# Kernel optimization log

Measured on AMD Instinct MI355X. Metric: run time of the kernel, lower is better.

The kernel has to match this reference:

```python
import jax, jax.numpy as jnp
import numpy as np

D = 1024
N_HEAD = 16
EXP = 4
EPS = 1e-6


def setup_inputs() -> dict:
    key = jax.random.key(0)
    ks = jax.random.split(key, 7)
    s = 0.02
    return {
        "x": jax.random.normal(ks[0], (2, 2048, D), dtype=jnp.float32),
        "w_qkv": jax.random.normal(ks[1], (3 * D, D), dtype=jnp.float32) * s,
        "w_o": jax.random.normal(ks[2], (D, D), dtype=jnp.float32) * s,
        "w_up": jax.random.normal(ks[3], (EXP * D, D), dtype=jnp.float32) * s,
        "w_gate": jax.random.normal(ks[4], (EXP * D, D), dtype=jnp.float32) * s,
        "w_down": jax.random.normal(ks[5], (D, EXP * D), dtype=jnp.float32) * s,
        "scale1": jnp.ones((D,), dtype=jnp.float32),
        "scale2": jnp.ones((D,), dtype=jnp.float32),
    }


def rmsnorm(x, scale):
    return x / jnp.sqrt(jnp.mean(x * x, axis=-1, keepdims=True) + EPS) * scale


def attention(x, w_qkv, w_o):
    b, s, d = x.shape
    dh = d // N_HEAD
    qkv = x @ w_qkv.T  # [b,s,3d]
    q, k, v = jnp.split(qkv, 3, axis=-1)
    # [b,h,s,dh]
    q = q.reshape(b, s, N_HEAD, dh).transpose(0, 2, 1, 3)
    k = k.reshape(b, s, N_HEAD, dh).transpose(0, 2, 1, 3)
    v = v.reshape(b, s, N_HEAD, dh).transpose(0, 2, 1, 3)
    scores = jnp.einsum("bhqd,bhkd->bhqk", q, k) / jnp.sqrt(jnp.float32(dh))
    causal = jnp.tril(jnp.ones((s, s), dtype=bool))
    scores = jnp.where(causal, scores, -jnp.inf)
    attn = jax.nn.softmax(scores, axis=-1)
    out = jnp.einsum("bhqk,bhkd->bhqd", attn, v)
    out = out.transpose(0, 2, 1, 3).reshape(b, s, d)
    return out @ w_o.T


def mlp(x, w_up, w_gate, w_down):
    return (x @ w_up.T * jax.nn.silu(x @ w_gate.T)) @ w_down.T


def reference(x, w_qkv, w_o, w_up, w_gate, w_down, scale1, scale2):
    x = x + attention(rmsnorm(x, scale1), w_qkv, w_o)
    return x + mlp(rmsnorm(x, scale2), w_up, w_gate, w_down)
```

## Files before the change

### kernel.cpp

```cpp
#include <hip/hip_runtime.h>


typedef __attribute__((ext_vector_type(8))) short short8;
typedef __attribute__((ext_vector_type(4))) float floatx4;

#define EPI_NONE 0
#define EPI_RES  1
#define EPI_GATE 2
#define EPI_QKV  3

#define QSCALE 0.1803368801f

__device__ __forceinline__ float b2f(unsigned short u) {
  union { unsigned int i; float f; } c; c.i = ((unsigned int)u) << 16; return c.f;
}
__device__ __forceinline__ unsigned short f2b(float f) {
  union { float f; unsigned int u; } c; c.f = f;
  unsigned int r = 0x7fffu + ((c.u >> 16) & 1u);
  return (unsigned short)((c.u + r) >> 16);
}
__device__ __forceinline__ unsigned int f2b2(float a, float b) {
  return (unsigned int)f2b(a) | ((unsigned int)f2b(b) << 16);
}

__device__ __forceinline__ void load_lds16(const void* g, void* l) {
  __builtin_amdgcn_global_load_lds(
      (const __attribute__((address_space(1))) unsigned int*)g,
      (__attribute__((address_space(3))) unsigned int*)l, 16, 0, 0);
}

__global__ __launch_bounds__(256)
void cvt_all_kernel(const float* __restrict__ wq, const float* __restrict__ wo,
                    const float* __restrict__ wu, const float* __restrict__ wg,
                    const float* __restrict__ wd,
                    unsigned short* __restrict__ oq, unsigned short* __restrict__ oo,
                    unsigned short* __restrict__ ou, unsigned short* __restrict__ og,
                    unsigned short* __restrict__ od) {
  int i = blockIdx.x * 256 + threadIdx.x;
  const float* src; unsigned short* dst; int k;
  if (i < 786432)        { src = wq; dst = oq; k = i; }
  else if (i < 1048576)  { src = wo; dst = oo; k = i - 786432; }
  else if (i < 2097152)  { src = wu; dst = ou; k = i - 1048576; }
  else if (i < 3145728)  { src = wg; dst = og; k = i - 2097152; }
  else                   { src = wd; dst = od; k = i - 3145728; }
  float4 v = ((const float4*)src)[k];
  ushort4 o;
  o.x = f2b(v.x); o.y = f2b(v.y); o.z = f2b(v.z); o.w = f2b(v.w);
  ((ushort4*)dst)[k] = o;
}

__global__ __launch_bounds__(256)
void rmsnorm_kernel(const float* __restrict__ x,
                    const float* __restrict__ scale,
                    unsigned short* __restrict__ y) {
  const int row = blockIdx.x;
  const int tid = threadIdx.x;
  const int base = row * 1024 + tid * 4;
  float4 v = *(const float4*)(x + base);
  float ss = v.x*v.x + v.y*v.y + v.z*v.z + v.w*v.w;
#pragma unroll
  for (int d = 32; d > 0; d >>= 1) ss += __shfl_down(ss, d);
  __shared__ float red[4];
  const int wave = tid >> 6, lane = tid & 63;
  if (lane == 0) red[wave] = ss;
  __syncthreads();
  float tot = red[0] + red[1] + red[2] + red[3];
  float rs = rsqrtf(tot * (1.0f/1024.0f) + 1e-6f);
  float4 sv = *(const float4*)(scale + tid * 4);
  ushort4 o;
  o.x = f2b(v.x * rs * sv.x);
  o.y = f2b(v.y * rs * sv.y);
  o.z = f2b(v.z * rs * sv.z);
  o.w = f2b(v.w * rs * sv.w);
  *(ushort4*)(y + base) = o;
}

__global__ __launch_bounds__(256)
void rmsnorm_res2_kernel(const float* __restrict__ x,
                         const float* __restrict__ p0,
                         const float* __restrict__ p1,
                         const float* __restrict__ scale,
                         float* __restrict__ x1,
                         unsigned short* __restrict__ y) {
  const int row = blockIdx.x;
  const int tid = threadIdx.x;
  const int base = row * 1024 + tid * 4;
  float4 a = *(const float4*)(x + base);
  float4 b = *(const float4*)(p0 + base);
  float4 c = *(const float4*)(p1 + base);
  float4 v;
  v.x = a.x + b.x + c.x; v.y = a.y + b.y + c.y;
  v.z = a.z + b.z + c.z; v.w = a.w + b.w + c.w;
  *(float4*)(x1 + base) = v;
  float ss = v.x*v.x + v.y*v.y + v.z*v.z + v.w*v.w;
#pragma unroll
  for (int d = 32; d > 0; d >>= 1) ss += __shfl_down(ss, d);
  __shared__ float red[4];
  const int wave = tid >> 6, lane = tid & 63;
  if (lane == 0) red[wave] = ss;
  __syncthreads();
  float tot = red[0] + red[1] + red[2] + red[3];
  float rs = rsqrtf(tot * (1.0f/1024.0f) + 1e-6f);
  float4 sv = *(const float4*)(scale + tid * 4);
  ushort4 o;
  o.x = f2b(v.x * rs * sv.x);
  o.y = f2b(v.y * rs * sv.y);
  o.z = f2b(v.z * rs * sv.z);
  o.w = f2b(v.w * rs * sv.w);
  *(ushort4*)(y + base) = o;
}

__global__ __launch_bounds__(256)
void reduce_out_kernel(const float* __restrict__ x1,
                       const float* __restrict__ p1,
                       float* outp) {
  int i = blockIdx.x * 256 + threadIdx.x;
  float4 a = ((const float4*)x1)[i];
  float4 b = ((const float4*)p1)[i];
  float4 c = ((float4*)outp)[i];
  float4 v;
  v.x = a.x + b.x + c.x; v.y = a.y + b.y + c.y;
  v.z = a.z + b.z + c.z; v.w = a.w + b.w + c.w;
  ((float4*)outp)[i] = v;
}

template<int EPI, typename OutT, typename ResT>
__global__ __launch_bounds__(256)
void gemm_bt(const unsigned short* __restrict__ A,
             const unsigned short* __restrict__ B,
             OutT* C, const ResT* R, unsigned short* VT,
             int M, int N, int K, int ldc) {
  __shared__ __align__(16) unsigned short As[128 * 32];
  __shared__ __align__(16) unsigned short Bs[128 * 32];
  const int tid = threadIdx.x;
  const int wave = tid >> 6;
  const int lane = tid & 63;
  const int m0 = blockIdx.y * 128;
  const int n0 = blockIdx.x * 128;
  const int wm = (wave & 1) * 64;
  const int wn = (wave >> 1) * 64;
  const int frow = lane & 15;
  const int fk = (lane >> 4) * 8;

  floatx4 acc[4][4];
#pragma unroll
  for (int i = 0; i < 4; ++i)
#pragma unroll
    for (int j = 0; j < 4; ++j) acc[i][j] = (floatx4){0.f, 0.f, 0.f, 0.f};

  const int srow = lane >> 2;
  const int scol = (lane & 3) * 8;
  const unsigned short* Ag  = A + (size_t)(m0 + wave * 16 + srow) * K + scol;
  const unsigned short* Ag2 = A + (size_t)(m0 + (wave + 4) * 16 + srow) * K + scol;
  const unsigned short* Bg  = B + (size_t)(n0 + wave * 16 + srow) * K + scol;
  const unsigned short* Bg2 = B + (size_t)(n0 + (wave + 4) * 16 + srow) * K + scol;

  for (int k0 = 0; k0 < K; k0 += 32) {
    __syncthreads();
    load_lds16(Ag + k0,  &As[wave * 512]);
    load_lds16(Ag2 + k0, &As[(wave + 4) * 512]);
    load_lds16(Bg + k0,  &Bs[wave * 512]);
    load_lds16(Bg2 + k0, &Bs[(wave + 4) * 512]);
    __syncthreads();
    short8 af[4], bf[4];
#pragma unroll
    for (int i = 0; i < 4; ++i) af[i] = *(const short8*)&As[(wm + 16*i + frow)*32 + fk];
#pragma unroll
    for (int j = 0; j < 4; ++j) bf[j] = *(const short8*)&Bs[(wn + 16*j + frow)*32 + fk];
#pragma unroll
    for (int i = 0; i < 4; ++i)
#pragma unroll
      for (int j = 0; j < 4; ++j)
        acc[i][j] = __builtin_amdgcn_mfma_f32_16x16x32_bf16(af[i], bf[j], acc[i][j], 0, 0, 0);
  }

  const int g4 = (lane >> 4) * 4;

  if constexpr (EPI == EPI_QKV) {
    if (n0 >= 2048) {
#pragma unroll
      for (int i = 0; i < 4; ++i) {
        const int row0 = m0 + wm + 16*i + g4;
        const int b = row0 >> 11, s0 = row0 & 2047;
#pragma unroll
        for (int j = 0; j < 4; ++j) {
          const int col = n0 + wn + 16*j + frow;
          const int dg = col - 2048;
          const int rowv = (b << 10) + dg;
          ushort4 ov;
          ov.x = f2b(acc[i][j][0]);
          ov.y = f2b(acc[i][j][1]);
          ov.z = f2b(acc[i][j][2]);
          ov.w = f2b(acc[i][j][3]);
          *(ushort4*)(VT + (size_t)rowv * 2048 + s0) = ov;
        }
      }
      return;
    }
  }

  const float qs = (EPI == EPI_QKV && n0 < 1024) ? QSCALE : 1.0f;
#pragma unroll
  for (int i = 0; i < 4; ++i) {
#pragma unroll
    for (int r = 0; r < 4; ++r) {
      const int row = m0 + wm + 16*i + g4 + r;
#pragma unroll
      for (int j = 0; j < 4; ++j) {
        const int col = n0 + wn + 16*j + frow;
        const size_t idx = (size_t)row * ldc + col;
        float v = acc[i][j][r];
        if constexpr (EPI == EPI_RES) {
          v += (float)R[idx];
        } else if constexpr (EPI == EPI_GATE) {
          float up = b2f((unsigned short)R[idx]);
          v = up * (v / (1.f + __expf(-v)));
        } else if constexpr (EPI == EPI_QKV) {
          v *= qs;
        }
        if constexpr (sizeof(OutT) == 4) C[idx] = v;
        else                             C[idx] = f2b(v);
      }
    }
  }
}

__global__ __launch_bounds__(256)
void gemm_bt_splitk(const unsigned short* __restrict__ A,
                    const unsigned short* __restrict__ B,
                    float* __restrict__ P0, float* __restrict__ P1,
                    int M, int N, int K, int Ks) {
  __shared__ __align__(16) unsigned short As[128 * 32];
  __shared__ __align__(16) unsigned short Bs[128 * 32];
  const int tid = threadIdx.x;
  const int wave = tid >> 6;
  const int lane = tid & 63;
  const int m0 = blockIdx.y * 128;
  const int n0 = blockIdx.x * 128;
  const int z = blockIdx.z;
  float* C = z ? P1 : P0;
  const int kbase = z * Ks;
  const int wm = (wave & 1) * 64;
  const int wn = (wave >> 1) * 64;
  const int frow = lane & 15;
  const int fk = (lane >> 4) * 8;

  floatx4 acc[4][4];
#pragma unroll
  for (int i = 0; i < 4; ++i)
#pragma unroll
    for (int j = 0; j < 4; ++j) acc[i][j] = (floatx4){0.f, 0.f, 0.f, 0.f};

  const int srow = lane >> 2;
  const int scol = (lane & 3) * 8;
  const unsigned short* Ag  = A + (size_t)(m0 + wave * 16 + srow) * K + kbase + scol;
  const unsigned short* Ag2 = A + (size_t)(m0 + (wave + 4) * 16 + srow) * K + kbase + scol;
  const unsigned short* Bg  = B + (size_t)(n0 + wave * 16 + srow) * K + kbase + scol;
  const unsigned short* Bg2 = B + (size_t)(n0 + (wave + 4) * 16 + srow) * K + kbase + scol;

  for (int k0 = 0; k0 < Ks; k0 += 32) {
    __syncthreads();
    load_lds16(Ag + k0,  &As[wave * 512]);
    load_lds16(Ag2 + k0, &As[(wave + 4) * 512]);
    load_lds16(Bg + k0,  &Bs[wave * 512]);
    load_lds16(Bg2 + k0, &Bs[(wave + 4) * 512]);
    __syncthreads();
    short8 af[4], bf[4];
#pragma unroll
    for (int i = 0; i < 4; ++i) af[i] = *(const short8*)&As[(wm + 16*i + frow)*32 + fk];
#pragma unroll
    for (int j = 0; j < 4; ++j) bf[j] = *(const short8*)&Bs[(wn + 16*j + frow)*32 + fk];
#pragma unroll
    for (int i = 0; i < 4; ++i)
#pragma unroll
      for (int j = 0; j < 4; ++j)
        acc[i][j] = __builtin_amdgcn_mfma_f32_16x16x32_bf16(af[i], bf[j], acc[i][j], 0, 0, 0);
  }

  const int g4 = (lane >> 4) * 4;
#pragma unroll
  for (int i = 0; i < 4; ++i)
#pragma unroll
    for (int r = 0; r < 4; ++r) {
      const int row = m0 + wm + 16*i + g4 + r;
#pragma unroll
      for (int j = 0; j < 4; ++j) {
        const int col = n0 + wn + 16*j + frow;
        C[(size_t)row * N + col] = acc[i][j][r];
      }
    }
}


#define A_OFF(q,h) (((q)*2+(h))*8192)
#define B_OFF(q,h) (32768 + ((q)*2+(h))*8192)

#define GBAR() __builtin_amdgcn_s_barrier()
#define WLG()  asm volatile("s_waitcnt lgkmcnt(0)" ::: "memory")
#define WVM(N) asm volatile("s_waitcnt vmcnt(" #N ")" ::: "memory")

#define STAGE(LB, SRC, T) do {                                               \
    const unsigned short* _s = (SRC) + (size_t)r0 * 1024 + (T) * 64 + gs;    \
    load_lds16(_s,             &lds[(LB) + wave * 512]);                     \
    load_lds16(_s + 64 * 1024, &lds[(LB) + 4096 + wave * 512]);              \
  } while (0)

#define LDA4(dst, q, h) do {                                                 \
    const unsigned short* _b = &lds[A_OFF(q,h) + arow];                      \
    _Pragma("unroll")                                                        \
    for (int _i = 0; _i < 4; ++_i) {                                         \
      dst[_i][0] = *(const short8*)(_b + _i * 1024 + g0);                    \
      dst[_i][1] = *(const short8*)(_b + _i * 1024 + g1);                    \
    }                                                                        \
  } while (0)

#define LDB2(dst, q, h) do {                                                 \
    const unsigned short* _b = &lds[B_OFF(q,h) + brow];                      \
    _Pragma("unroll")                                                        \
    for (int _j = 0; _j < 2; ++_j) {                                         \
      dst[_j][0] = *(const short8*)(_b + _j * 1024 + g0);                    \
      dst[_j][1] = *(const short8*)(_b + _j * 1024 + g1);                    \
    }                                                                        \
  } while (0)

#define MMQ(aa, bb, IO, JO) do {                                             \
    _Pragma("unroll")                                                        \
    for (int _i = 0; _i < 4; ++_i)                                           \
      _Pragma("unroll")                                                      \
      for (int _j = 0; _j < 2; ++_j) {                                       \
        acc[(IO)+_i][(JO)+_j] = __builtin_amdgcn_mfma_f32_16x16x32_bf16(     \
            aa[_i][0], bb[_j][0], acc[(IO)+_i][(JO)+_j], 0, 0, 0);           \
        acc[(IO)+_i][(JO)+_j] = __builtin_amdgcn_mfma_f32_16x16x32_bf16(     \
            aa[_i][1], bb[_j][1], acc[(IO)+_i][(JO)+_j], 0, 0, 0);           \
      }                                                                      \
  } while (0)

__global__ __launch_bounds__(512, 2)
void gemm256_upgate(const unsigned short* __restrict__ A,
                    const unsigned short* __restrict__ Bu,
                    const unsigned short* __restrict__ Bg,
                    unsigned short* __restrict__ C) {
  extern __shared__ __align__(16) unsigned short lds[];
  const int tid  = threadIdx.x;
  const int wave = tid >> 6;
  const int lane = tid & 63;
  const int wr   = wave >> 2;
  const int wc   = wave & 3;
  const int frow = lane & 15;
  const int s4   = lane >> 4;

  const int orig = blockIdx.x;
  const int swz  = (orig & 7) * 64 + (orig >> 3);
  const int bx   = swz & 31;
  const int by   = swz >> 5;
  const int m0   = by * 256;
  const int n0   = bx * 128;

  const int f7 = frow & 7;
  const int g0 = ((0 + s4) ^ f7) * 8;
  const int g1 = ((4 + s4) ^ f7) * 8;
  const int arow = (wr * 64 + frow) * 64;
  const int brow = (wc * 32 + frow) * 64;

  const int r0 = wave * 8 + (lane >> 3);
  const int gs = ((lane & 7) ^ (lane >> 3)) * 8;

  const unsigned short* Asrc  = A  + (size_t)m0 * 1024;
  const unsigned short* B0src = Bu + (size_t)(bx * 128) * 1024;
  const unsigned short* B1src = Bg + (size_t)(bx * 128) * 1024;

  floatx4 acc[8][4];
#pragma unroll
  for (int i = 0; i < 8; ++i)
#pragma unroll
    for (int j = 0; j < 4; ++j) acc[i][j] = (floatx4){0.f, 0.f, 0.f, 0.f};

  STAGE(A_OFF(0,0), Asrc, 0);
  STAGE(B_OFF(0,0), B0src, 0);
  STAGE(B_OFF(0,1), B1src, 0);
  STAGE(A_OFF(0,1), Asrc + 128 * 1024, 0);
  WVM(4);
  STAGE(A_OFF(1,0), Asrc, 1);
  STAGE(B_OFF(1,0), B0src, 1);
  STAGE(B_OFF(1,1), B1src, 1);
  WVM(6);
  GBAR();

  short8 af0[4][2], af1[4][2], bf0[2][2], bf1[2][2];

  for (int it = 0; it < 8; ++it) {
    const int t   = it * 2;
    const int tn2 = (t + 2) & 15;
    const int tn3 = (t + 3) & 15;
    LDA4(af0, 0, 0);
    LDB2(bf0, 0, 0);
    STAGE(A_OFF(1,1), Asrc + 128 * 1024, (t + 1) & 15);
    GBAR(); WLG();
    __builtin_amdgcn_s_setprio(1); MMQ(af0, bf0, 0, 0); __builtin_amdgcn_s_setprio(0);
    GBAR();
    LDB2(bf1, 0, 1);
    STAGE(A_OFF(0,0), Asrc, tn2);
    GBAR(); WLG();
    __builtin_amdgcn_s_setprio(1); MMQ(af0, bf1, 0, 2); __builtin_amdgcn_s_setprio(0);
    GBAR();
    LDA4(af1, 0, 1);
    STAGE(B_OFF(0,0), B0src, tn2);
    GBAR(); WLG();
    __builtin_amdgcn_s_setprio(1); MMQ(af1, bf0, 4, 0); __builtin_amdgcn_s_setprio(0);
    GBAR();
    STAGE(B_OFF(0,1), B1src, tn2);
    GBAR();
    __builtin_amdgcn_s_setprio(1); MMQ(af1, bf1, 4, 2); __builtin_amdgcn_s_setprio(0);
    WVM(6);
    GBAR();
    LDA4(af0, 1, 0);
    LDB2(bf0, 1, 0);
    STAGE(A_OFF(0,1), Asrc + 128 * 1024, tn2);
    GBAR(); WLG();
    __builtin_amdgcn_s_setprio(1); MMQ(af0, bf0, 0, 0); __builtin_amdgcn_s_setprio(0);
    GBAR();
    LDB2(bf1, 1, 1);
    STAGE(A_OFF(1,0), Asrc, tn3);
    GBAR(); WLG();
    __builtin_amdgcn_s_setprio(1); MMQ(af0, bf1, 0, 2); __builtin_amdgcn_s_setprio(0);
    GBAR();
    LDA4(af1, 1, 1);
    STAGE(B_OFF(1,0), B0src, tn3);
    GBAR(); WLG();
    __builtin_amdgcn_s_setprio(1); MMQ(af1, bf0, 4, 0); __builtin_amdgcn_s_setprio(0);
    GBAR();
    STAGE(B_OFF(1,1), B1src, tn3);
    GBAR();
    __builtin_amdgcn_s_setprio(1); MMQ(af1, bf1, 4, 2); __builtin_amdgcn_s_setprio(0);
    WVM(6);
    GBAR();
  }
  asm volatile("s_waitcnt vmcnt(0)" ::: "memory");

#pragma unroll
  for (int i = 0; i < 8; ++i) {
    const int row = m0 + (i >> 2) * 128 + wr * 64 + (i & 3) * 16 + s4 * 4;
#pragma unroll
    for (int j = 0; j < 2; ++j) {
      const int col = n0 + wc * 32 + j * 16 + frow;
#pragma unroll
      for (int r = 0; r < 4; ++r) {
        const float g = acc[i][j + 2][r];
        const float v = acc[i][j][r] * (g / (1.f + __expf(-g)));
        C[(size_t)(row + r) * 4096 + col] = f2b(v);
      }
    }
  }
}

__global__ __launch_bounds__(256, 2)
void attn_kernel(const unsigned short* __restrict__ qkv,
                 const unsigned short* __restrict__ vt,
                 unsigned short* __restrict__ out) {
  const int lin = blockIdx.x;
  const int bh = lin & 31;
  const int q_idx = lin >> 5;
  const int qblk = (q_idx < 8) ? (2 * q_idx) : (31 - 2 * q_idx);
  const int b = bh >> 4, h = bh & 15;
  const int tid = threadIdx.x, w = tid >> 6, lane = tid & 63;
  const int f = lane & 15, g = lane >> 4;
  const int fk = g * 8, g4 = g * 4;

  __shared__ __align__(16) unsigned short Ks[2][128 * 32];
  __shared__ __align__(16) unsigned short Vs[4][64 * 32];
  __shared__ __align__(16) unsigned int   pl[4][64 * 36];

  const unsigned short* Qb = qkv + (size_t)(b * 2048) * 2048 + h * 64;
  const unsigned short* Kb = Qb + 1024;
  const unsigned short* Vt = vt + ((size_t)(b * 16 + h) * 64) * 2048;

  const int q0 = qblk * 128 + w * 32;
  short8 qf[2][2];
#pragma unroll
  for (int i = 0; i < 2; ++i)
#pragma unroll
    for (int kq = 0; kq < 2; ++kq)
      qf[i][kq] = *(const short8*)(Qb + (size_t)(q0 + 16*i + f) * 2048 + kq * 32 + fk);

  float m_s[2] = {-1e30f, -1e30f}, l_s[2] = {0.f, 0.f};
  floatx4 o[4][2];
#pragma unroll
  for (int mt = 0; mt < 4; ++mt)
#pragma unroll
    for (int i = 0; i < 2; ++i) o[mt][i] = (floatx4){0.f, 0.f, 0.f, 0.f};

  const int srow = lane >> 2;
  const int scol = (lane & 3) * 8;
  unsigned int* plw = pl[w];

  for (int kb = 0; kb <= qblk; ++kb) {
    __syncthreads();
#pragma unroll
    for (int u = 0; u < 2; ++u) {
      const int seg = w + 4 * u;
#pragma unroll
      for (int kq = 0; kq < 2; ++kq)
        load_lds16(Kb + (size_t)(kb * 128 + seg * 16 + srow) * 2048 + kq * 32 + scol,
                   &Ks[kq][seg * 512]);
    }
#pragma unroll
    for (int c = 0; c < 4; ++c)
      load_lds16(Vt + (size_t)(w * 16 + srow) * 2048 + kb * 128 + c * 32 + scol,
                 &Vs[c][w * 512]);
    __syncthreads();

    const bool diag = (kb == qblk);
    const int jhi0 = diag ? 2 * w : 7;
    const int jhi1 = diag ? 2 * w + 1 : 7;

    floatx4 s[8][2];
#pragma unroll
    for (int j = 0; j < 8; ++j) {
      if (j > jhi1) continue;
      short8 kf0 = *(const short8*)&Ks[0][(16*j + f) * 32 + fk];
      short8 kf1 = *(const short8*)&Ks[1][(16*j + f) * 32 + fk];
#pragma unroll
      for (int i = 0; i < 2; ++i) {
        if (j > (i ? jhi1 : jhi0)) continue;
        s[j][i] = (floatx4){0.f, 0.f, 0.f, 0.f};
        s[j][i] = __builtin_amdgcn_mfma_f32_16x16x32_bf16(kf0, qf[i][0], s[j][i], 0, 0, 0);
        s[j][i] = __builtin_amdgcn_mfma_f32_16x16x32_bf16(kf1, qf[i][1], s[j][i], 0, 0, 0);
      }
    }
    if (diag) {
#pragma unroll
      for (int i = 0; i < 2; ++i) {
        const int qo = 32 * w + 16 * i + f;
        const int jh = i ? jhi1 : jhi0;
#pragma unroll
        for (int j = 0; j < 8; ++j) {
          if (j > jh) continue;
#pragma unroll
          for (int r = 0; r < 4; ++r)
            if (16 * j + g4 + r > qo) s[j][i][r] = -1e30f;
        }
      }
    }
#pragma unroll
    for (int i = 0; i < 2; ++i) {
      const int jh = i ? jhi1 : jhi0;
      float mx = -1e30f;
#pragma unroll
      for (int j = 0; j < 8; ++j) {
        if (j > jh) continue;
#pragma unroll
        for (int r = 0; r < 4; ++r) mx = fmaxf(mx, s[j][i][r]);
      }
      mx = fmaxf(mx, __shfl_xor(mx, 16));
      mx = fmaxf(mx, __shfl_xor(mx, 32));
      const float mnew = fmaxf(m_s[i], mx);
      const float alpha = exp2f(m_s[i] - mnew);
      float rs = 0.f;
#pragma unroll
      for (int j = 0; j < 8; ++j) {
        if (j > jh) continue;
#pragma unroll
        for (int r = 0; r < 4; ++r) {
          float pv = exp2f(s[j][i][r] - mnew);
          s[j][i][r] = pv;
          rs += pv;
        }
      }
      rs += __shfl_xor(rs, 16);
      rs += __shfl_xor(rs, 32);
      l_s[i] = l_s[i] * alpha + rs;
      m_s[i] = mnew;
#pragma unroll
      for (int mt = 0; mt < 4; ++mt) o[mt][i] *= alpha;
    }
#pragma unroll
    for (int i = 0; i < 2; ++i) {
      const int jh = i ? jhi1 : jhi0;
#pragma unroll
      for (int j = 0; j < 8; ++j) {
        if (j > jh) continue;
        plw[(8*j + 2*g + 0) * 36 + 16*i + f] = f2b2(s[j][i][0], s[j][i][1]);
        plw[(8*j + 2*g + 1) * 36 + 16*i + f] = f2b2(s[j][i][2], s[j][i][3]);
      }
    }
    if (diag) {
      plw[(8*(2*w + 1) + 2*g + 0) * 36 + f] = 0u;
      plw[(8*(2*w + 1) + 2*g + 1) * 36 + f] = 0u;
    }
    const int chi = diag ? w : 3;
#pragma unroll
    for (int c = 0; c < 4; ++c) {
      if (c > chi) continue;
      union { unsigned int d[4]; short8 v; } pb[2];
#pragma unroll
      for (int i = 0; i < 2; ++i)
#pragma unroll
        for (int k = 0; k < 4; ++k)
          pb[i].d[k] = plw[(16*c + 4*g + k) * 36 + 16*i + f];
#pragma unroll
      for (int mt = 0; mt < 4; ++mt) {
        short8 va = *(const short8*)&Vs[c][(16*mt + f) * 32 + fk];
#pragma unroll
        for (int i = 0; i < 2; ++i)
          o[mt][i] = __builtin_amdgcn_mfma_f32_16x16x32_bf16(va, pb[i].v, o[mt][i], 0, 0, 0);
      }
    }
  }

#pragma unroll
  for (int i = 0; i < 2; ++i) {
    const float inv = 1.0f / l_s[i];
    unsigned short* orow = out + (size_t)(b * 2048 + q0 + 16*i + f) * 1024 + h * 64;
#pragma unroll
    for (int mt = 0; mt < 4; ++mt) {
      ushort4 ov;
      ov.x = f2b(o[mt][i][0] * inv);
      ov.y = f2b(o[mt][i][1] * inv);
      ov.z = f2b(o[mt][i][2] * inv);
      ov.w = f2b(o[mt][i][3] * inv);
      *(ushort4*)(orow + 16 * mt + g4) = ov;
    }
  }
}

extern "C" void kernel_launch(void* const* d_in, const int* in_sizes, int n_in,
                              void* d_out, int out_size, void* d_ws, size_t ws_size,
                              hipStream_t stream) {
  const float* x      = (const float*)d_in[0];
  const float* w_qkv  = (const float*)d_in[1];
  const float* w_o    = (const float*)d_in[2];
  const float* w_up   = (const float*)d_in[3];
  const float* w_gate = (const float*)d_in[4];
  const float* w_down = (const float*)d_in[5];
  const float* scale1 = (const float*)d_in[6];
  const float* scale2 = (const float*)d_in[7];

  char* ws = (char*)d_ws;
  unsigned short* wq_b = (unsigned short*)(ws);
  unsigned short* wo_b = (unsigned short*)(ws +  6291456);
  unsigned short* wu_b = (unsigned short*)(ws +  8388608);
  unsigned short* wg_b = (unsigned short*)(ws + 16777216);
  unsigned short* wd_b = (unsigned short*)(ws + 25165824);
  unsigned short* qkv  = (unsigned short*)(ws + 33554432);
  unsigned short* hup  = (unsigned short*)(ws + 33554432);
  unsigned short* vT   = (unsigned short*)(ws + 50331648);
  unsigned short* attnb= (unsigned short*)(ws + 58720256);
  unsigned short* xn   = (unsigned short*)(ws + 67108864);
  float*          x1   = (float*)         (ws + 75497472);
  float*          outp = (float*)d_out;

  float* wo_p0   = (float*)(ws + 33554432);
  float* wo_p1   = (float*)d_out;
  float* down_p0 = (float*)d_out;
  float* down_p1 = (float*)(ws + 8388608);

  const int M = 4096;
  dim3 blk(256);

  static int lds_opted = 0;
  if (!lds_opted) {
    hipFuncSetAttribute((const void*)gemm256_upgate,
                        hipFuncAttributeMaxDynamicSharedMemorySize, 131072);
    lds_opted = 1;
  }

  cvt_all_kernel<<<16384, blk, 0, stream>>>(w_qkv, w_o, w_up, w_gate, w_down,
                                            wq_b, wo_b, wu_b, wg_b, wd_b);

  rmsnorm_kernel<<<4096, blk, 0, stream>>>(x, scale1, xn);
  gemm_bt<EPI_QKV, unsigned short, unsigned short>
      <<<dim3(24, 32), blk, 0, stream>>>(xn, wq_b, qkv, (const unsigned short*)nullptr, vT,
                                         M, 3072, 1024, 2048);
  attn_kernel<<<dim3(512), blk, 0, stream>>>(qkv, vT, attnb);
  gemm_bt_splitk<<<dim3(8, 32, 2), blk, 0, stream>>>(attnb, wo_b, wo_p0, wo_p1,
                                                     M, 1024, 1024, 512);

  rmsnorm_res2_kernel<<<4096, blk, 0, stream>>>(x, wo_p0, wo_p1, scale2, x1, xn);

  gemm256_upgate<<<dim3(512), dim3(512), 131072, stream>>>(xn, wu_b, wg_b, hup);
  gemm_bt_splitk<<<dim3(8, 32, 2), blk, 0, stream>>>(hup, wd_b, down_p0, down_p1,
                                                     M, 1024, 4096, 2048);
  reduce_out_kernel<<<4096, blk, 0, stream>>>(x1, down_p1, outp);

  (void)in_sizes; (void)n_in; (void)out_size; (void)ws_size;
}
```

Measured before the change: 416.9 us.

## Read attention K/V straight from global memory and pair query blocks per workgroup

```diff
diff --git a/kernel.cpp b/kernel.cpp
--- a/kernel.cpp
+++ b/kernel.cpp
@@ -453,22 +453,21 @@
   }
 }
 
-__global__ __launch_bounds__(256, 2)
+__global__ __launch_bounds__(512, 2)
 void attn_kernel(const unsigned short* __restrict__ qkv,
                  const unsigned short* __restrict__ vt,
                  unsigned short* __restrict__ out) {
-  const int lin = blockIdx.x;
-  const int bh = lin & 31;
-  const int q_idx = lin >> 5;
-  const int qblk = (q_idx < 8) ? (2 * q_idx) : (31 - 2 * q_idx);
+  extern __shared__ __align__(16) unsigned int pl[];
+  const int bh = blockIdx.x & 31;
+  const int qi = blockIdx.x >> 5;
   const int b = bh >> 4, h = bh & 15;
-  const int tid = threadIdx.x, w = tid >> 6, lane = tid & 63;
+  const int tid = threadIdx.x;
+  const int gw = tid >> 6;
+  const int w = gw & 3;
+  const int qblk = (gw < 4) ? (2 * qi) : (15 - 2 * qi);
+  const int lane = tid & 63;
   const int f = lane & 15, g = lane >> 4;
   const int fk = g * 8, g4 = g * 4;
-
-  __shared__ __align__(16) unsigned short Ks[2][128 * 32];
-  __shared__ __align__(16) unsigned short Vs[4][64 * 32];
-  __shared__ __align__(16) unsigned int   pl[4][64 * 36];
 
   const unsigned short* Qb = qkv + (size_t)(b * 2048) * 2048 + h * 64;
   const unsigned short* Kb = Qb + 1024;
@@ -489,25 +488,11 @@
 #pragma unroll
     for (int i = 0; i < 2; ++i) o[mt][i] = (floatx4){0.f, 0.f, 0.f, 0.f};
 
-  const int srow = lane >> 2;
-  const int scol = (lane & 3) * 8;
-  unsigned int* plw = pl[w];
+  unsigned int* plw = pl + gw * (64 * 36);
 
   for (int kb = 0; kb <= qblk; ++kb) {
-    __syncthreads();
-#pragma unroll
-    for (int u = 0; u < 2; ++u) {
-      const int seg = w + 4 * u;
-#pragma unroll
-      for (int kq = 0; kq < 2; ++kq)
-        load_lds16(Kb + (size_t)(kb * 128 + seg * 16 + srow) * 2048 + kq * 32 + scol,
-                   &Ks[kq][seg * 512]);
-    }
-#pragma unroll
-    for (int c = 0; c < 4; ++c)
-      load_lds16(Vt + (size_t)(w * 16 + srow) * 2048 + kb * 128 + c * 32 + scol,
-                 &Vs[c][w * 512]);
-    __syncthreads();
+    const unsigned short* Kt = Kb + (size_t)(kb * 128) * 2048 + fk;
+    const unsigned short* Vc = Vt + kb * 128 + fk;
 
     const bool diag = (kb == qblk);
     const int jhi0 = diag ? 2 * w : 7;
@@ -517,8 +502,10 @@
 #pragma unroll
     for (int j = 0; j < 8; ++j) {
       if (j > jhi1) continue;
-      short8 kf0 = *(const short8*)&Ks[0][(16*j + f) * 32 + fk];
-      short8 kf1 = *(const short8*)&Ks[1][(16*j + f) * 32 + fk];
+      const unsigned short* Kr = Kt + (size_t)(16*j + f) * 2048;
+      short8 kf0 = *(const short8*)(Kr);
+      short8 kf1 = *(const short8*)(Kr + 32);
+      __builtin_amdgcn_s_setprio(1);
 #pragma unroll
       for (int i = 0; i < 2; ++i) {
         if (j > (i ? jhi1 : jhi0)) continue;
@@ -526,6 +513,7 @@
         s[j][i] = __builtin_amdgcn_mfma_f32_16x16x32_bf16(kf0, qf[i][0], s[j][i], 0, 0, 0);
         s[j][i] = __builtin_amdgcn_mfma_f32_16x16x32_bf16(kf1, qf[i][1], s[j][i], 0, 0, 0);
       }
+      __builtin_amdgcn_s_setprio(0);
     }
     if (diag) {
 #pragma unroll
@@ -599,10 +587,12 @@
           pb[i].d[k] = plw[(16*c + 4*g + k) * 36 + 16*i + f];
 #pragma unroll
       for (int mt = 0; mt < 4; ++mt) {
-        short8 va = *(const short8*)&Vs[c][(16*mt + f) * 32 + fk];
+        short8 va = *(const short8*)(Vc + (size_t)(16*mt + f) * 2048 + c * 32);
+        __builtin_amdgcn_s_setprio(1);
 #pragma unroll
         for (int i = 0; i < 2; ++i)
           o[mt][i] = __builtin_amdgcn_mfma_f32_16x16x32_bf16(va, pb[i].v, o[mt][i], 0, 0, 0);
+        __builtin_amdgcn_s_setprio(0);
       }
     }
   }
@@ -661,6 +651,8 @@
   if (!lds_opted) {
     hipFuncSetAttribute((const void*)gemm256_upgate,
                         hipFuncAttributeMaxDynamicSharedMemorySize, 131072);
+    hipFuncSetAttribute((const void*)attn_kernel,
+                        hipFuncAttributeMaxDynamicSharedMemorySize, 73728);
     lds_opted = 1;
   }
 
@@ -671,7 +663,7 @@
   gemm_bt<EPI_QKV, unsigned short, unsigned short>
       <<<dim3(24, 32), blk, 0, stream>>>(xn, wq_b, qkv, (const unsigned short*)nullptr, vT,
                                          M, 3072, 1024, 2048);
-  attn_kernel<<<dim3(512), blk, 0, stream>>>(qkv, vT, attnb);
+  attn_kernel<<<dim3(256), dim3(512), 73728, stream>>>(qkv, vT, attnb);
   gemm_bt_splitk<<<dim3(8, 32, 2), blk, 0, stream>>>(attnb, wo_b, wo_p0, wo_p1,
                                                      M, 1024, 1024, 512);
 
```

New measurement: 477.2 us. 14.5% more time.

## Double-buffer attention K/V tiles, swizzle LDS, and pass P via permlane swaps

Applied to the files above, without the earlier changes.

```diff
diff --git a/kernel.cpp b/kernel.cpp
--- a/kernel.cpp
+++ b/kernel.cpp
@@ -28,6 +28,10 @@
       (const __attribute__((address_space(1))) unsigned int*)g,
       (__attribute__((address_space(3))) unsigned int*)l, 16, 0, 0);
 }
+
+#define GBAR() __builtin_amdgcn_s_barrier()
+#define WLG()  asm volatile("s_waitcnt lgkmcnt(0)" ::: "memory")
+#define WVM(N) asm volatile("s_waitcnt vmcnt(" #N ")" ::: "memory")
 
 __global__ __launch_bounds__(256)
 void cvt_all_kernel(const float* __restrict__ wq, const float* __restrict__ wo,
@@ -295,10 +299,6 @@
 #define A_OFF(q,h) (((q)*2+(h))*8192)
 #define B_OFF(q,h) (32768 + ((q)*2+(h))*8192)
 
-#define GBAR() __builtin_amdgcn_s_barrier()
-#define WLG()  asm volatile("s_waitcnt lgkmcnt(0)" ::: "memory")
-#define WVM(N) asm volatile("s_waitcnt vmcnt(" #N ")" ::: "memory")
-
 #define STAGE(LB, SRC, T) do {                                               \
     const unsigned short* _s = (SRC) + (size_t)r0 * 1024 + (T) * 64 + gs;    \
     load_lds16(_s,             &lds[(LB) + wave * 512]);                     \
@@ -457,6 +457,8 @@
 void attn_kernel(const unsigned short* __restrict__ qkv,
                  const unsigned short* __restrict__ vt,
                  unsigned short* __restrict__ out) {
+  __shared__ __align__(16) unsigned short Ks[2][2][128 * 32];
+  __shared__ __align__(16) unsigned short Vs[2][4][64 * 32];
   const int lin = blockIdx.x;
   const int bh = lin & 31;
   const int q_idx = lin >> 5;
@@ -465,10 +467,7 @@
   const int tid = threadIdx.x, w = tid >> 6, lane = tid & 63;
   const int f = lane & 15, g = lane >> 4;
   const int fk = g * 8, g4 = g * 4;
-
-  __shared__ __align__(16) unsigned short Ks[2][128 * 32];
-  __shared__ __align__(16) unsigned short Vs[4][64 * 32];
-  __shared__ __align__(16) unsigned int   pl[4][64 * 36];
+  const int fks = (g ^ ((f >> 1) & 3)) * 8;
 
   const unsigned short* Qb = qkv + (size_t)(b * 2048) * 2048 + h * 64;
   const unsigned short* Kb = Qb + 1024;
@@ -490,24 +489,36 @@
     for (int i = 0; i < 2; ++i) o[mt][i] = (floatx4){0.f, 0.f, 0.f, 0.f};
 
   const int srow = lane >> 2;
-  const int scol = (lane & 3) * 8;
-  unsigned int* plw = pl[w];
-
-  for (int kb = 0; kb <= qblk; ++kb) {
-    __syncthreads();
+  const int scolx = ((lane & 3) ^ ((lane >> 3) & 3)) * 8;
+
+  auto stage = [&](int bb, int kb) {
 #pragma unroll
     for (int u = 0; u < 2; ++u) {
       const int seg = w + 4 * u;
 #pragma unroll
       for (int kq = 0; kq < 2; ++kq)
-        load_lds16(Kb + (size_t)(kb * 128 + seg * 16 + srow) * 2048 + kq * 32 + scol,
-                   &Ks[kq][seg * 512]);
+        load_lds16(Kb + (size_t)(kb * 128 + seg * 16 + srow) * 2048 + kq * 32 + scolx,
+                   &Ks[bb][kq][seg * 512]);
     }
 #pragma unroll
     for (int c = 0; c < 4; ++c)
-      load_lds16(Vt + (size_t)(w * 16 + srow) * 2048 + kb * 128 + c * 32 + scol,
-                 &Vs[c][w * 512]);
-    __syncthreads();
+      load_lds16(Vt + (size_t)(w * 16 + srow) * 2048 + kb * 128 + c * 32 + scolx,
+                 &Vs[bb][c][w * 512]);
+  };
+
+  stage(0, 0);
+
+  for (int kb = 0; kb <= qblk; ++kb) {
+    const int cur = kb & 1;
+    GBAR();
+    if (kb < qblk) {
+      stage(cur ^ 1, kb + 1);
+      WVM(8);
+    } else {
+      WVM(0);
+    }
+    GBAR();
+    __builtin_amdgcn_sched_barrier(0);
 
     const bool diag = (kb == qblk);
     const int jhi0 = diag ? 2 * w : 7;
@@ -517,8 +528,9 @@
 #pragma unroll
     for (int j = 0; j < 8; ++j) {
       if (j > jhi1) continue;
-      short8 kf0 = *(const short8*)&Ks[0][(16*j + f) * 32 + fk];
-      short8 kf1 = *(const short8*)&Ks[1][(16*j + f) * 32 + fk];
+      short8 kf0 = *(const short8*)&Ks[cur][0][(16*j + f) * 32 + fks];
+      short8 kf1 = *(const short8*)&Ks[cur][1][(16*j + f) * 32 + fks];
+      __builtin_amdgcn_s_setprio(1);
 #pragma unroll
       for (int i = 0; i < 2; ++i) {
         if (j > (i ? jhi1 : jhi0)) continue;
@@ -526,6 +538,7 @@
         s[j][i] = __builtin_amdgcn_mfma_f32_16x16x32_bf16(kf0, qf[i][0], s[j][i], 0, 0, 0);
         s[j][i] = __builtin_amdgcn_mfma_f32_16x16x32_bf16(kf1, qf[i][1], s[j][i], 0, 0, 0);
       }
+      __builtin_amdgcn_s_setprio(0);
     }
     if (diag) {
 #pragma unroll
@@ -573,36 +586,38 @@
 #pragma unroll
       for (int mt = 0; mt < 4; ++mt) o[mt][i] *= alpha;
     }
-#pragma unroll
-    for (int i = 0; i < 2; ++i) {
-      const int jh = i ? jhi1 : jhi0;
-#pragma unroll
-      for (int j = 0; j < 8; ++j) {
-        if (j > jh) continue;
-        plw[(8*j + 2*g + 0) * 36 + 16*i + f] = f2b2(s[j][i][0], s[j][i][1]);
-        plw[(8*j + 2*g + 1) * 36 + 16*i + f] = f2b2(s[j][i][2], s[j][i][3]);
-      }
-    }
-    if (diag) {
-      plw[(8*(2*w + 1) + 2*g + 0) * 36 + f] = 0u;
-      plw[(8*(2*w + 1) + 2*g + 1) * 36 + f] = 0u;
-    }
+
     const int chi = diag ? w : 3;
 #pragma unroll
     for (int c = 0; c < 4; ++c) {
       if (c > chi) continue;
-      union { unsigned int d[4]; short8 v; } pb[2];
-#pragma unroll
-      for (int i = 0; i < 2; ++i)
-#pragma unroll
-        for (int k = 0; k < 4; ++k)
-          pb[i].d[k] = plw[(16*c + 4*g + k) * 36 + 16*i + f];
+      short8 pb[2];
+#pragma unroll
+      for (int i = 0; i < 2; ++i) {
+        const int jh = i ? jhi1 : jhi0;
+        unsigned int P01 = f2b2(s[2*c][i][0], s[2*c][i][1]);
+        unsigned int P23 = f2b2(s[2*c][i][2], s[2*c][i][3]);
+        unsigned int Q01 = 0u, Q23 = 0u;
+        if (2*c + 1 <= jh) {
+          Q01 = f2b2(s[2*c+1][i][0], s[2*c+1][i][1]);
+          Q23 = f2b2(s[2*c+1][i][2], s[2*c+1][i][3]);
+        }
+        asm("v_permlane32_swap_b32 %0, %1" : "+v"(P01), "+v"(Q01));
+        asm("v_permlane32_swap_b32 %0, %1" : "+v"(P23), "+v"(Q23));
+        asm("v_permlane16_swap_b32 %0, %1" : "+v"(P01), "+v"(Q01));
+        asm("v_permlane16_swap_b32 %0, %1" : "+v"(P23), "+v"(Q23));
+        union { unsigned int d[4]; short8 v; } pbu;
+        pbu.d[0] = P01; pbu.d[1] = P23; pbu.d[2] = Q01; pbu.d[3] = Q23;
+        pb[i] = pbu.v;
+      }
 #pragma unroll
       for (int mt = 0; mt < 4; ++mt) {
-        short8 va = *(const short8*)&Vs[c][(16*mt + f) * 32 + fk];
+        short8 va = *(const short8*)&Vs[cur][c][(16*mt + f) * 32 + fks];
+        __builtin_amdgcn_s_setprio(1);
 #pragma unroll
         for (int i = 0; i < 2; ++i)
-          o[mt][i] = __builtin_amdgcn_mfma_f32_16x16x32_bf16(va, pb[i].v, o[mt][i], 0, 0, 0);
+          o[mt][i] = __builtin_amdgcn_mfma_f32_16x16x32_bf16(va, pb[i], o[mt][i], 0, 0, 0);
+        __builtin_amdgcn_s_setprio(0);
       }
     }
   }
@@ -659,8 +674,8 @@
 
   static int lds_opted = 0;
   if (!lds_opted) {
-    hipFuncSetAttribute((const void*)gemm256_upgate,
-                        hipFuncAttributeMaxDynamicSharedMemorySize, 131072);
+    (void)hipFuncSetAttribute((const void*)gemm256_upgate,
+                              hipFuncAttributeMaxDynamicSharedMemorySize, 131072);
     lds_opted = 1;
   }
 
```

After: 403.2 us. 3.3% less time.
